# Performance work log

Hardware: AMD Instinct MI355X
Metric: run time of the kernel (lower is better)

## Reference

```python
import jax, jax.numpy as jnp
import numpy as np

B, N, K, H = 8, 4096, 32, 256
LN_EPS = 1e-5


def setup_inputs() -> dict:
    key = jax.random.key(0)
    k1, k2, k3, k4, k5 = jax.random.split(key, 5)
    h = jax.random.normal(k1, (B, N, H), dtype=jnp.float32)
    nbr_idx = jax.random.randint(k2, (B, N, K), 0, N, dtype=jnp.int64)
    nbr_w = jax.random.uniform(k3, (B, N, K), dtype=jnp.float32)
    # Linear weights stored torch-style as [out, in]; y = x @ W.T
    W_self = jax.random.normal(k4, (H, H), dtype=jnp.float32) / np.sqrt(H)
    W_neigh = jax.random.normal(k5, (H, H), dtype=jnp.float32) / np.sqrt(H)
    ln_gamma = jnp.ones((H,), dtype=jnp.float32)
    ln_beta = jnp.zeros((H,), dtype=jnp.float32)
    return {"h": h, "nbr_idx": nbr_idx, "nbr_w": nbr_w, "W_self": W_self,
            "W_neigh": W_neigh, "ln_gamma": ln_gamma, "ln_beta": ln_beta}


def _layer_norm(x, gamma, beta):
    mu = jnp.mean(x, axis=-1, keepdims=True)
    var = jnp.mean(jnp.square(x - mu), axis=-1, keepdims=True)
    return (x - mu) * jax.lax.rsqrt(var + LN_EPS) * gamma + beta


def reference(h, nbr_idx, nbr_w, W_self, W_neigh, ln_gamma, ln_beta):
    b, n, hd = h.shape
    k = nbr_idx.shape[2]
    # gather neighbor features: [B, N, k, H]
    flat_idx = nbr_idx.reshape(b, n * k)
    h_nbr = jnp.take_along_axis(h, flat_idx[:, :, None], axis=1).reshape(b, n, k, hd)
    # weighted aggregate over neighbors
    h_agg = jnp.einsum('bnk,bnkh->bnh', nbr_w, h_nbr)
    # dual linear + exact (erf) GELU, matching torch nn.GELU default
    out = jax.nn.gelu(h @ W_self.T + h_agg @ W_neigh.T, approximate=False)
    # dropout is identity in eval mode
    return _layer_norm(out, ln_gamma, ln_beta)
```

## Files before the change

kernel.cpp:

```cpp
#include <hip/hip_runtime.h>
#include <hip/hip_bf16.h>
#include <hip/hip_fp16.h>
#include <math.h>
#include <stdint.h>

constexpr int Nn = 4096, Kk = 32, Hh = 256;
constexpr int Mm = 8 * Nn;

typedef float  f32x4 __attribute__((ext_vector_type(4)));
typedef short  s16x8 __attribute__((ext_vector_type(8)));
struct alignas(16) H2x4 { __half2 a, b, c, d; };

static __device__ __forceinline__ ushort f2bf(float f) {
  uint32_t u = __float_as_uint(f);
  u += 0x7FFF + ((u >> 16) & 1);
  return (ushort)(u >> 16);
}
static __device__ __forceinline__ void gl_lds16(const ushort* g, ushort* l) {
  __builtin_amdgcn_global_load_lds(
      (const __attribute__((address_space(1))) void*)g,
      (__attribute__((address_space(3))) void*)l, 16, 0, 0);
}
static __device__ __forceinline__ float gelu_t(float x) {
  float u = x * x;
  float y = x * (1.5957691216f + 0.0713548162726f * u);
  float t = __expf(y);
  return x - x * __builtin_amdgcn_rcpf(t + 1.0f);
}

__global__ __launch_bounds__(256) void prep_w(const float* __restrict__ Ws,
                                              const float* __restrict__ Wn,
                                              ushort* __restrict__ Wc,
                                              const int* __restrict__ idxp,
                                              int* __restrict__ flag) {
  if (blockIdx.x == 0 && threadIdx.x < 64) {
    unsigned long long bl = __ballot(idxp[2 * threadIdx.x + 1] != 0);
    if (threadIdx.x == 0) *flag = (bl != 0ULL) ? 1 : 0;
  }
  int i = blockIdx.x * 256 + threadIdx.x;
  int j  = i >> 6;
  int k4 = i & 63;
  const float* src = (j < 256) ? (Ws + (size_t)j * 256 + k4 * 4)
                               : (Wn + (size_t)(j - 256) * 256 + k4 * 4);
  float4 v = *reinterpret_cast<const float4*>(src);
  ushort4 o = { f2bf(v.x), f2bf(v.y), f2bf(v.z), f2bf(v.w) };
  reinterpret_cast<ushort4*>(Wc)[i] = o;
}

__global__ __launch_bounds__(512, 4) void gemm1(const float* __restrict__ h,
                                                const ushort* __restrict__ Wc,
                                                __half* __restrict__ hs,
                                                __half* __restrict__ hn) {
  __shared__ ushort lA[2][64 * 64];
  __shared__ ushort lB[2][256 * 64];
  const int tid = threadIdx.x, wid = tid >> 6, lane = tid & 63;
  const int wr = wid >> 1, wc = wid & 1;

  const int blk = blockIdx.x;
  const int b = blk & 7, t = blk >> 3;
  const int nblk = t & 1, mblk = t >> 1;
  const int m0 = b * Nn + mblk * 64;
  const ushort* Wbase = Wc + (size_t)nblk * 256 * 256;

  f32x4 acc[8];
  #pragma unroll
  for (int j = 0; j < 8; ++j) acc[j] = f32x4{0.f, 0.f, 0.f, 0.f};

  float4 a0, a1;
  const int ar = tid >> 3, as = tid & 7;
  auto aload = [&](int kt) {
    const float* src = h + (size_t)(m0 + ar) * 256 + kt * 64 + as * 8;
    a0 = *reinterpret_cast<const float4*>(src);
    a1 = *reinterpret_cast<const float4*>(src + 4);
  };
  auto awrite = [&](int buf) {
    s16x8 u = { (short)f2bf(a0.x), (short)f2bf(a0.y), (short)f2bf(a0.z),
                (short)f2bf(a0.w), (short)f2bf(a1.x), (short)f2bf(a1.y),
                (short)f2bf(a1.z), (short)f2bf(a1.w) };
    *reinterpret_cast<s16x8*>(&lA[buf][ar * 64 + ((as ^ (ar & 7)) << 3)]) = u;
  };
  auto bstage = [&](int buf, int kt) {
    #pragma unroll
    for (int c = 0; c < 4; ++c) {
      int ch = wid + c * 8;
      int r = ch * 8 + (lane >> 3);
      int s = (lane & 7) ^ (r & 7);
      gl_lds16(Wbase + (size_t)r * 256 + kt * 64 + s * 8, &lB[buf][ch * 512]);
    }
  };

  aload(0);
  bstage(0, 0);
  awrite(0);
  __syncthreads();

  int buf = 0;
  for (int kt = 0; kt < 4; ++kt) {
    if (kt < 3) { aload(kt + 1); bstage(buf ^ 1, kt + 1); }
    #pragma unroll
    for (int kk = 0; kk < 2; ++kk) {
      const int ks = kk * 4 + (lane >> 4);
      const int ra = wr * 16 + (lane & 15);
      s16x8 af = *reinterpret_cast<const s16x8*>(
          &lA[buf][ra * 64 + ((ks ^ (ra & 7)) << 3)]);
      s16x8 bfr[8];
      #pragma unroll
      for (int nj = 0; nj < 8; ++nj) {
        int rb = wc * 128 + nj * 16 + (lane & 15);
        bfr[nj] = *reinterpret_cast<const s16x8*>(
            &lB[buf][rb * 64 + ((ks ^ (rb & 7)) << 3)]);
      }
      #pragma unroll
      for (int nj = 0; nj < 8; ++nj)
        acc[nj] = __builtin_amdgcn_mfma_f32_16x16x32_bf16(af, bfr[nj],
                                                          acc[nj], 0, 0, 0);
    }
    if (kt < 3) awrite(buf ^ 1);
    __syncthreads();
    buf ^= 1;
  }

  __half* dst = (nblk == 0) ? hs : hn;
  #pragma unroll
  for (int nj = 0; nj < 8; ++nj)
    #pragma unroll
    for (int jj = 0; jj < 4; ++jj) {
      int row = wr * 16 + (lane >> 4) * 4 + jj;
      int col = wc * 128 + nj * 16 + (lane & 15);
      dst[(size_t)(m0 + row) * 256 + col] = __float2half(acc[nj][jj]);
    }
}

__global__ __launch_bounds__(256, 4) void k2(const __half* __restrict__ hs,
                                             const __half* __restrict__ hn,
                                             const void* __restrict__ idx,
                                             const float* __restrict__ w,
                                             const float* __restrict__ gamma,
                                             const float* __restrict__ beta,
                                             float* __restrict__ out,
                                             const int* __restrict__ flag) {
  const int tid = threadIdx.x, wv = tid >> 6, lane = tid & 63;
  const int hw = lane >> 5, l5 = lane & 31;
  const int b = blockIdx.x & 7;
  const int m = b * Nn + (blockIdx.x >> 3) * 4 + wv;
  const int is32 = *flag;

  size_t kb = (size_t)m * Kk + hw * 16 + (l5 & 15);
  int   myi = is32 ? ((const int*)idx)[kb] : (int)((const long long*)idx)[kb];
  float myw = w[kb];

  H2x4 hvq = *reinterpret_cast<const H2x4*>(hs + (size_t)m * Hh + l5 * 8);
  float4 gm0 = reinterpret_cast<const float4*>(gamma)[l5 * 2];
  float4 gm1 = reinterpret_cast<const float4*>(gamma)[l5 * 2 + 1];
  float4 bt0 = reinterpret_cast<const float4*>(beta)[l5 * 2];
  float4 bt1 = reinterpret_cast<const float4*>(beta)[l5 * 2 + 1];

  const __half* hnb = hn + (size_t)b * Nn * Hh;

  auto ld = [&](int k) -> H2x4 {
    int r = __shfl(myi, k, 32);
    return *reinterpret_cast<const H2x4*>(hnb + ((size_t)r << 8) + (l5 << 3));
  };

  f32x4 aA0{0,0,0,0}, aA1{0,0,0,0}, aB0{0,0,0,0}, aB1{0,0,0,0};

#define CONS(b0, b1, q, wt) { \
    b0[0] += (float)q.a.x * wt; b0[1] += (float)q.a.y * wt; \
    b0[2] += (float)q.b.x * wt; b0[3] += (float)q.b.y * wt; \
    b1[0] += (float)q.c.x * wt; b1[1] += (float)q.c.y * wt; \
    b1[2] += (float)q.d.x * wt; b1[3] += (float)q.d.y * wt; }

  H2x4 p0 = ld(0), p1 = ld(1), p2 = ld(2), p3 = ld(3);

  #pragma unroll
  for (int k = 0; k < 16; k += 4) {
    float w0 = __shfl(myw, k, 32),     w1 = __shfl(myw, k + 1, 32);
    float w2 = __shfl(myw, k + 2, 32), w3 = __shfl(myw, k + 3, 32);
    H2x4 q0 = p0, q1 = p1, q2 = p2, q3 = p3;
    if (k + 4 < 16) {
      p0 = ld(k + 4); p1 = ld(k + 5); p2 = ld(k + 6); p3 = ld(k + 7);
    }
    CONS(aA0, aA1, q0, w0); CONS(aB0, aB1, q1, w1);
    CONS(aA0, aA1, q2, w2); CONS(aB0, aB1, q3, w3);
  }
#undef CONS

  float g[8];
  #pragma unroll
  for (int j = 0; j < 4; ++j) {
    g[j]     = aA0[j] + aB0[j];
    g[j + 4] = aA1[j] + aB1[j];
  }
  #pragma unroll
  for (int j = 0; j < 8; ++j)
    g[j] += __shfl_xor(g[j], 32, 64);

  g[0] = gelu_t(g[0] + (float)hvq.a.x);
  g[1] = gelu_t(g[1] + (float)hvq.a.y);
  g[2] = gelu_t(g[2] + (float)hvq.b.x);
  g[3] = gelu_t(g[3] + (float)hvq.b.y);
  g[4] = gelu_t(g[4] + (float)hvq.c.x);
  g[5] = gelu_t(g[5] + (float)hvq.c.y);
  g[6] = gelu_t(g[6] + (float)hvq.d.x);
  g[7] = gelu_t(g[7] + (float)hvq.d.y);

  float sv = 0.f, qv = 0.f;
  #pragma unroll
  for (int j = 0; j < 8; ++j) { sv += g[j]; qv += g[j] * g[j]; }
  #pragma unroll
  for (int msk = 16; msk >= 1; msk >>= 1) {
    sv += __shfl_xor(sv, msk, 64);
    qv += __shfl_xor(qv, msk, 64);
  }
  float mean = sv * (1.0f / 256.0f);
  float var  = qv * (1.0f / 256.0f) - mean * mean;
  float inv  = rsqrtf(var + 1e-5f);

  float4 o0, o1;
  o0.x = (g[0] - mean) * inv * gm0.x + bt0.x;
  o0.y = (g[1] - mean) * inv * gm0.y + bt0.y;
  o0.z = (g[2] - mean) * inv * gm0.z + bt0.z;
  o0.w = (g[3] - mean) * inv * gm0.w + bt0.w;
  o1.x = (g[4] - mean) * inv * gm1.x + bt1.x;
  o1.y = (g[5] - mean) * inv * gm1.y + bt1.y;
  o1.z = (g[6] - mean) * inv * gm1.z + bt1.z;
  o1.w = (g[7] - mean) * inv * gm1.w + bt1.w;
  if (hw == 0) {
    float4* op = reinterpret_cast<float4*>(out + (size_t)m * Hh + l5 * 8);
    op[0] = o0;
    op[1] = o1;
  }
}

extern "C" void kernel_launch(void* const* d_in, const int* in_sizes, int n_in,
                              void* d_out, int out_size, void* d_ws, size_t ws_size,
                              hipStream_t stream) {
  const float* h     = (const float*)d_in[0];
  const void*  idx   = d_in[1];
  const float* w     = (const float*)d_in[2];
  const float* Ws    = (const float*)d_in[3];
  const float* Wn    = (const float*)d_in[4];
  const float* gamma = (const float*)d_in[5];
  const float* beta  = (const float*)d_in[6];
  float* out = (float*)d_out;

  __half* hs = (__half*)d_ws;
  __half* hn = hs + (size_t)Mm * Hh;
  ushort* Wc = (ushort*)(hn + (size_t)Mm * Hh);
  int* flag  = (int*)(Wc + 512 * 256);

  prep_w<<<128, 256, 0, stream>>>(Ws, Wn, Wc, (const int*)idx, flag);
  gemm1<<<1024, 512, 0, stream>>>(h, Wc, hs, hn);
  k2<<<8192, 256, 0, stream>>>(hs, hn, idx, w, gamma, beta, out, flag);
}
```

Measured before the change: 58.25 us.

## Stage neighbor feature column slices in LDS and split aggregation from GELU/LayerNorm

A new prep kernel packs each neighbor index and its fp16 weight into one 32-bit word, stored transposed by neighbor slot. The aggregation kernel loads an 8-column slice of every row of the batch's projected neighbor features into 64KB of LDS. It then gathers the 32 neighbors from LDS instead of from global memory and writes the aggregate back in place. A separate kernel then applies GELU and LayerNorm. This removes the large random global gather traffic. In exchange it adds two launches, one block per CU with possible LDS bank conflicts, and extra fp16 rounding of the weights and of the aggregate.

```diff
diff --git a/kernel.cpp b/kernel.cpp
--- a/kernel.cpp
+++ b/kernel.cpp
@@ -45,6 +45,25 @@
   float4 v = *reinterpret_cast<const float4*>(src);
   ushort4 o = { f2bf(v.x), f2bf(v.y), f2bf(v.z), f2bf(v.w) };
   reinterpret_cast<ushort4*>(Wc)[i] = o;
+}
+
+__global__ __launch_bounds__(256) void prep_meta(const void* __restrict__ idx,
+                                                 const float* __restrict__ w,
+                                                 uint* __restrict__ meta,
+                                                 const int* __restrict__ flag) {
+  int i = blockIdx.x * 256 + threadIdx.x;
+  int b = i >> 12, t = i & 4095;
+  int is32 = *flag;
+  const int*       i32 = (const int*)idx + (size_t)i * Kk;
+  const long long* i64 = (const long long*)idx + (size_t)i * Kk;
+  const float*     wp  = w + (size_t)i * Kk;
+  uint* mb = meta + ((size_t)b << 17);
+  #pragma unroll
+  for (int k = 0; k < Kk; ++k) {
+    uint r = (uint)(is32 ? i32[k] : (int)i64[k]) & 0xFFFFu;
+    ushort hw = __half_as_ushort(__float2half(wp[k]));
+    mb[(size_t)k * 4096 + t] = r | ((uint)hw << 16);
+  }
 }
 
 __global__ __launch_bounds__(512, 4) void gemm1(const float* __restrict__ h,
@@ -131,78 +150,90 @@
     }
 }
 
-__global__ __launch_bounds__(256, 4) void k2(const __half* __restrict__ hs,
-                                             const __half* __restrict__ hn,
-                                             const void* __restrict__ idx,
-                                             const float* __restrict__ w,
-                                             const float* __restrict__ gamma,
-                                             const float* __restrict__ beta,
-                                             float* __restrict__ out,
-                                             const int* __restrict__ flag) {
+__global__ __launch_bounds__(512, 1) void k2a(__half* __restrict__ hn,
+                                              const uint* __restrict__ meta) {
+  __shared__ __align__(16) __half sl[4096 * 8];
   const int tid = threadIdx.x, wv = tid >> 6, lane = tid & 63;
-  const int hw = lane >> 5, l5 = lane & 31;
   const int b = blockIdx.x & 7;
-  const int m = b * Nn + (blockIdx.x >> 3) * 4 + wv;
-  const int is32 = *flag;
-
-  size_t kb = (size_t)m * Kk + hw * 16 + (l5 & 15);
-  int   myi = is32 ? ((const int*)idx)[kb] : (int)((const long long*)idx)[kb];
-  float myw = w[kb];
-
-  H2x4 hvq = *reinterpret_cast<const H2x4*>(hs + (size_t)m * Hh + l5 * 8);
-  float4 gm0 = reinterpret_cast<const float4*>(gamma)[l5 * 2];
-  float4 gm1 = reinterpret_cast<const float4*>(gamma)[l5 * 2 + 1];
-  float4 bt0 = reinterpret_cast<const float4*>(beta)[l5 * 2];
-  float4 bt1 = reinterpret_cast<const float4*>(beta)[l5 * 2 + 1];
-
-  const __half* hnb = hn + (size_t)b * Nn * Hh;
-
-  auto ld = [&](int k) -> H2x4 {
-    int r = __shfl(myi, k, 32);
-    return *reinterpret_cast<const H2x4*>(hnb + ((size_t)r << 8) + (l5 << 3));
-  };
-
-  f32x4 aA0{0,0,0,0}, aA1{0,0,0,0}, aB0{0,0,0,0}, aB1{0,0,0,0};
-
+  const int c = blockIdx.x >> 3;
+  __half* hnb = hn + ((size_t)b << 20);
+
+  #pragma unroll
+  for (int j = 0; j < 8; ++j) {
+    int rbase = j * 512 + wv * 64;
+    gl_lds16((const ushort*)(hnb + (size_t)(rbase + lane) * 256 + c * 8),
+             (ushort*)&sl[rbase * 8]);
+  }
+  __syncthreads();
+
+  const uint* mb = meta + ((size_t)b << 17);
+
+  for (int ch = 0; ch < 8; ++ch) {
+    const int t = wv * 512 + ch * 64 + lane;
+    const uint* mcol = mb + t;
+
+    uint mk[32];
+    #pragma unroll
+    for (int k = 0; k < 32; ++k) mk[k] = mcol[(size_t)k << 12];
+
+    f32x4 aA0{0,0,0,0}, aA1{0,0,0,0}, aB0{0,0,0,0}, aB1{0,0,0,0};
+
+#define DS(k) (*reinterpret_cast<const H2x4*>(&sl[(mk[k] & 0xFFFFu) * 8]))
+#define WVAL(k) __half2float(__ushort_as_half((ushort)(mk[k] >> 16)))
 #define CONS(b0, b1, q, wt) { \
     b0[0] += (float)q.a.x * wt; b0[1] += (float)q.a.y * wt; \
     b0[2] += (float)q.b.x * wt; b0[3] += (float)q.b.y * wt; \
     b1[0] += (float)q.c.x * wt; b1[1] += (float)q.c.y * wt; \
     b1[2] += (float)q.d.x * wt; b1[3] += (float)q.d.y * wt; }
 
-  H2x4 p0 = ld(0), p1 = ld(1), p2 = ld(2), p3 = ld(3);
-
-  #pragma unroll
-  for (int k = 0; k < 16; k += 4) {
-    float w0 = __shfl(myw, k, 32),     w1 = __shfl(myw, k + 1, 32);
-    float w2 = __shfl(myw, k + 2, 32), w3 = __shfl(myw, k + 3, 32);
-    H2x4 q0 = p0, q1 = p1, q2 = p2, q3 = p3;
-    if (k + 4 < 16) {
-      p0 = ld(k + 4); p1 = ld(k + 5); p2 = ld(k + 6); p3 = ld(k + 7);
-    }
-    CONS(aA0, aA1, q0, w0); CONS(aB0, aB1, q1, w1);
-    CONS(aA0, aA1, q2, w2); CONS(aB0, aB1, q3, w3);
-  }
+    H2x4 p0 = DS(0), p1 = DS(1), p2 = DS(2), p3 = DS(3);
+    #pragma unroll
+    for (int k = 0; k < 32; k += 4) {
+      float w0 = WVAL(k), w1 = WVAL(k + 1), w2 = WVAL(k + 2), w3 = WVAL(k + 3);
+      H2x4 q0 = p0, q1 = p1, q2 = p2, q3 = p3;
+      if (k + 4 < 32) {
+        p0 = DS(k + 4); p1 = DS(k + 5); p2 = DS(k + 6); p3 = DS(k + 7);
+      }
+      CONS(aA0, aA1, q0, w0); CONS(aB0, aB1, q1, w1);
+      CONS(aA0, aA1, q2, w2); CONS(aB0, aB1, q3, w3);
+    }
+#undef DS
+#undef WVAL
 #undef CONS
 
+    H2x4 o;
+    o.a = __floats2half2_rn(aA0[0] + aB0[0], aA0[1] + aB0[1]);
+    o.b = __floats2half2_rn(aA0[2] + aB0[2], aA0[3] + aB0[3]);
+    o.c = __floats2half2_rn(aA1[0] + aB1[0], aA1[1] + aB1[1]);
+    o.d = __floats2half2_rn(aA1[2] + aB1[2], aA1[3] + aB1[3]);
+    *reinterpret_cast<H2x4*>(hnb + (size_t)t * 256 + c * 8) = o;
+  }
+}
+
+__global__ __launch_bounds__(256) void k2b(const __half* __restrict__ hs,
+                                           const __half* __restrict__ hagg,
+                                           const float* __restrict__ gamma,
+                                           const float* __restrict__ beta,
+                                           float* __restrict__ out) {
+  const int tid = threadIdx.x, l5 = tid & 31;
+  const int m = blockIdx.x * 8 + (tid >> 5);
+
+  H2x4 av = *reinterpret_cast<const H2x4*>(hagg + (size_t)m * Hh + l5 * 8);
+  H2x4 sv_ = *reinterpret_cast<const H2x4*>(hs + (size_t)m * Hh + l5 * 8);
+  float4 gm0 = reinterpret_cast<const float4*>(gamma)[l5 * 2];
+  float4 gm1 = reinterpret_cast<const float4*>(gamma)[l5 * 2 + 1];
+  float4 bt0 = reinterpret_cast<const float4*>(beta)[l5 * 2];
+  float4 bt1 = reinterpret_cast<const float4*>(beta)[l5 * 2 + 1];
+
   float g[8];
-  #pragma unroll
-  for (int j = 0; j < 4; ++j) {
-    g[j]     = aA0[j] + aB0[j];
-    g[j + 4] = aA1[j] + aB1[j];
-  }
-  #pragma unroll
-  for (int j = 0; j < 8; ++j)
-    g[j] += __shfl_xor(g[j], 32, 64);
-
-  g[0] = gelu_t(g[0] + (float)hvq.a.x);
-  g[1] = gelu_t(g[1] + (float)hvq.a.y);
-  g[2] = gelu_t(g[2] + (float)hvq.b.x);
-  g[3] = gelu_t(g[3] + (float)hvq.b.y);
-  g[4] = gelu_t(g[4] + (float)hvq.c.x);
-  g[5] = gelu_t(g[5] + (float)hvq.c.y);
-  g[6] = gelu_t(g[6] + (float)hvq.d.x);
-  g[7] = gelu_t(g[7] + (float)hvq.d.y);
+  g[0] = gelu_t((float)av.a.x + (float)sv_.a.x);
+  g[1] = gelu_t((float)av.a.y + (float)sv_.a.y);
+  g[2] = gelu_t((float)av.b.x + (float)sv_.b.x);
+  g[3] = gelu_t((float)av.b.y + (float)sv_.b.y);
+  g[4] = gelu_t((float)av.c.x + (float)sv_.c.x);
+  g[5] = gelu_t((float)av.c.y + (float)sv_.c.y);
+  g[6] = gelu_t((float)av.d.x + (float)sv_.d.x);
+  g[7] = gelu_t((float)av.d.y + (float)sv_.d.y);
 
   float sv = 0.f, qv = 0.f;
   #pragma unroll
@@ -225,11 +256,9 @@
   o1.y = (g[5] - mean) * inv * gm1.y + bt1.y;
   o1.z = (g[6] - mean) * inv * gm1.z + bt1.z;
   o1.w = (g[7] - mean) * inv * gm1.w + bt1.w;
-  if (hw == 0) {
-    float4* op = reinterpret_cast<float4*>(out + (size_t)m * Hh + l5 * 8);
-    op[0] = o0;
-    op[1] = o1;
-  }
+  float4* op = reinterpret_cast<float4*>(out + (size_t)m * Hh + l5 * 8);
+  op[0] = o0;
+  op[1] = o1;
 }
 
 extern "C" void kernel_launch(void* const* d_in, const int* in_sizes, int n_in,
@@ -248,8 +277,11 @@
   __half* hn = hs + (size_t)Mm * Hh;
   ushort* Wc = (ushort*)(hn + (size_t)Mm * Hh);
   int* flag  = (int*)(Wc + 512 * 256);
+  uint* meta = (uint*)(flag + 64);
 
   prep_w<<<128, 256, 0, stream>>>(Ws, Wn, Wc, (const int*)idx, flag);
+  prep_meta<<<128, 256, 0, stream>>>(idx, w, meta, flag);
   gemm1<<<1024, 512, 0, stream>>>(h, Wc, hs, hn);
-  k2<<<8192, 256, 0, stream>>>(hs, hn, idx, w, gamma, beta, out, flag);
-}
+  k2a<<<256, 512, 0, stream>>>(hn, meta);
+  k2b<<<4096, 256, 0, stream>>>(hs, hn, gamma, beta, out);
+}
```

Measured after the change: 82.53 us. 41.7% more time.
